# Kernel optimization log

Measured on AMD Instinct MI355X. Metric: run time of the kernel, lower is better.

Reference implementation:

```python
import jax, jax.numpy as jnp
import numpy as np

GROUPS = 32
NUM_HEADS = 8
EPS = 1e-5


def setup_inputs() -> dict:
    key = jax.random.key(0)
    ks = jax.random.split(key, 8)
    b, c, h, w = 2, 256, 64, 64
    x = jax.random.normal(ks[0], (b, c, h, w), dtype=jnp.float32)
    gn_w = jnp.ones((c,), dtype=jnp.float32)
    gn_b = jnp.zeros((c,), dtype=jnp.float32)
    qkv_w = jax.random.normal(ks[1], (3 * c, c), dtype=jnp.float32) * 0.02  # 1x1 conv
    qkv_b = jnp.zeros((3 * c,), dtype=jnp.float32)
    proj_w = jax.random.normal(ks[2], (c, c), dtype=jnp.float32) * 0.02  # 1x1 conv
    proj_b = jnp.zeros((c,), dtype=jnp.float32)
    return {"x": x, "gn_w": gn_w, "gn_b": gn_b, "qkv_w": qkv_w,
            "qkv_b": qkv_b, "proj_w": proj_w, "proj_b": proj_b}


def _group_norm(x, w, b):
    bsz, c, h, wd = x.shape
    xg = x.reshape(bsz, GROUPS, c // GROUPS, h * wd)
    mean = jnp.mean(xg, axis=(2, 3), keepdims=True)
    var = jnp.mean(jnp.square(xg - mean), axis=(2, 3), keepdims=True)
    xn = ((xg - mean) * jax.lax.rsqrt(var + EPS)).reshape(bsz, c, h, wd)
    return xn * w[None, :, None, None] + b[None, :, None, None]


def reference(x, gn_w, gn_b, qkv_w, qkv_b, proj_w, proj_b):
    b, c, h, w = x.shape
    hd = c // NUM_HEADS
    s = h * w
    xn = _group_norm(x, gn_w, gn_b)
    # 1x1 conv == channel matmul
    qkv = jnp.einsum('oc,bcs->bos', qkv_w, xn.reshape(b, c, s)) + qkv_b[None, :, None]
    qkv = qkv.reshape(b, 3, NUM_HEADS, hd, s)
    q, k, v = qkv[:, 0], qkv[:, 1], qkv[:, 2]  # (b, nh, hd, s)
    scale = 1.0 / jnp.sqrt(jnp.asarray(hd, dtype=x.dtype))
    scores = jnp.einsum('bhds,bhdt->bhst', q, k) * scale  # (b, nh, s, s)
    attn = jax.nn.softmax(scores, axis=-1)
    out = jnp.einsum('bhst,bhdt->bhds', attn, v)  # (b, nh, hd, s)
    out = out.reshape(b, c, h, w)
    out = jnp.einsum('oc,bcs->bos', proj_w, out.reshape(b, c, s)).reshape(b, c, h, w)
    out = out + proj_b[None, :, None, None]
    return out + x
```

## Files before the change

### kernel.cpp

```cpp
#include <hip/hip_runtime.h>
#include <hip/hip_bf16.h>

#define B_ 2
#define C_ 256
#define S_ 4096
#define NH 8
#define HD 32
#define EPSV 1e-5f
#define QSC2 0.25503487942324256f

typedef __bf16 bf16_t;
typedef bf16_t bf16x8 __attribute__((ext_vector_type(8)));
typedef float f32x4 __attribute__((ext_vector_type(4)));
typedef float f32x16 __attribute__((ext_vector_type(16)));
typedef int i32x2 __attribute__((ext_vector_type(2)));
typedef __hip_bfloat16 hbf;

__device__ inline unsigned cvtpk_bf16(float a, float b) {
  unsigned r;
  asm("v_cvt_pk_bf16_f32 %0, %1, %2" : "=v"(r) : "v"(a), "v"(b));
  return r;
}

#if __has_builtin(__builtin_amdgcn_exp2f)
#define EXP2R(x) __builtin_amdgcn_exp2f(x)
#else
#define EXP2R(x) exp2f(x)
#endif

__global__ __launch_bounds__(256) void prep_kernel(const float* __restrict__ qkv_w,
                                                   const float* __restrict__ proj_w,
                                                   const float* __restrict__ x,
                                                   hbf* __restrict__ qkv_wf, hbf* __restrict__ proj_wf,
                                                   float* __restrict__ stats) {
  int blk = blockIdx.x;
  if (blk < 128) {
    const float* src = (blk < 96) ? qkv_w : proj_w;
    hbf* dst = (blk < 96) ? qkv_wf : proj_wf;
    int i = (blk < 96 ? blk : blk - 96) * 256 + threadIdx.x;
    int nchunks = (blk < 96) ? 768 * 32 : 256 * 32;
    if (i < nchunks) {
      int o = i >> 5, c8 = (i & 31) * 8;
      alignas(16) hbf tmp[8];
#pragma unroll
      for (int j = 0; j < 8; j++) tmp[j] = __float2bfloat16(src[(size_t)o * C_ + c8 + j]);
      *(uint4*)&dst[(((size_t)(o >> 5) * 16) + (c8 >> 4)) * 512 + (o & 31) * 16 + (c8 & 15)] = *(uint4*)tmp;
    }
    return;
  }
  int sb = blk - 128;
  int bg = sb >> 3, chunk = sb & 7;
  const float4* xp4 = (const float4*)(x + (size_t)bg * 8 * S_);
  float sum = 0.f, sumsq = 0.f;
#pragma unroll
  for (int p = 0; p < 4; p++) {
    int i = threadIdx.x + p * 256;
    int ch = i >> 7, s4 = i & 127;
    float4 v = xp4[ch * (S_ >> 2) + chunk * 128 + s4];
    sum += v.x + v.y + v.z + v.w;
    sumsq += v.x * v.x + v.y * v.y + v.z * v.z + v.w * v.w;
  }
#pragma unroll
  for (int off = 32; off > 0; off >>= 1) {
    sum += __shfl_down(sum, off);
    sumsq += __shfl_down(sumsq, off);
  }
  __shared__ float red[2][4];
  int wid = threadIdx.x >> 6;
  if ((threadIdx.x & 63) == 0) { red[0][wid] = sum; red[1][wid] = sumsq; }
  __syncthreads();
  if (threadIdx.x == 0) {
    stats[sb * 2 + 0] = red[0][0] + red[0][1] + red[0][2] + red[0][3];
    stats[sb * 2 + 1] = red[1][0] + red[1][1] + red[1][2] + red[1][3];
  }
}

__global__ __launch_bounds__(256) void gn_apply(const float* __restrict__ x, const float* __restrict__ gw,
                                                const float* __restrict__ gb, const float* __restrict__ stats,
                                                hbf* __restrict__ xn) {
  int bg = blockIdx.x >> 3, chunk = blockIdx.x & 7;
  int b = bg >> 5, g = bg & 31;
  const float* xp = x + (size_t)bg * 8 * S_;
  float sum = 0.f, sumsq = 0.f;
#pragma unroll
  for (int k = 0; k < 8; k++) {
    sum += stats[(bg * 8 + k) * 2 + 0];
    sumsq += stats[(bg * 8 + k) * 2 + 1];
  }
  const float inv_n = 1.f / (8 * S_);
  float mean = sum * inv_n;
  float rstd = rsqrtf(fmaxf(sumsq * inv_n - mean * mean, 0.f) + EPSV);
  float scv[8], shv[8];
#pragma unroll
  for (int c = 0; c < 8; c++) {
    scv[c] = gw[g * 8 + c] * rstd;
    shv[c] = gb[g * 8 + c] - mean * scv[c];
  }
#pragma unroll
  for (int p = 0; p < 2; p++) {
    int s = chunk * 512 + p * 256 + threadIdx.x;
    alignas(16) hbf tmp[8];
#pragma unroll
    for (int c = 0; c < 8; c++)
      tmp[c] = __float2bfloat16(xp[(size_t)c * S_ + s] * scv[c] + shv[c]);
    *(uint4*)&xn[(((size_t)b * (S_ >> 5) + (s >> 5)) * 16 + (g >> 1)) * 512 + (s & 31) * 16 + (g & 1) * 8] =
        *(uint4*)tmp;
  }
}

__global__ __launch_bounds__(512, 4) void qkv_gemm(const hbf* __restrict__ xn, const hbf* __restrict__ wf,
                                                   const float* __restrict__ bias,
                                                   hbf* __restrict__ qbuf, hbf* __restrict__ kg,
                                                   hbf* __restrict__ vg) {
  int bt = blockIdx.z;
  int m0 = blockIdx.x * 128;
  int n0 = blockIdx.y * 128;
  int tid = threadIdx.x, lane = tid & 63, w = tid >> 6;
  int wq = w & 3, wo = w >> 2;
  int l31 = lane & 31, hi = lane >> 5;
  const int loff = l31 * 16 + hi * 8;
  const hbf* ap = xn + ((size_t)bt * (S_ >> 5) + (m0 >> 5) + wq) * 8192;
  int oc0 = n0 + wo * 64;
  const hbf* bp0 = wf + (size_t)(oc0 >> 5) * 8192;
  const hbf* bp1 = bp0 + 8192;
  f32x16 acc0 = {0.f,0.f,0.f,0.f,0.f,0.f,0.f,0.f,0.f,0.f,0.f,0.f,0.f,0.f,0.f,0.f};
  f32x16 acc1 = acc0;
#pragma unroll 4
  for (int ks = 0; ks < 16; ++ks) {
    bf16x8 af = *(const bf16x8*)(ap + ks * 512 + loff);
    bf16x8 b0 = *(const bf16x8*)(bp0 + ks * 512 + loff);
    bf16x8 b1 = *(const bf16x8*)(bp1 + ks * 512 + loff);
    acc0 = __builtin_amdgcn_mfma_f32_32x32x16_bf16(af, b0, acc0, 0, 0, 0);
    acc1 = __builtin_amdgcn_mfma_f32_32x32x16_bf16(af, b1, acc1, 0, 0, 0);
  }
  int s_base = m0 + wq * 32;
#pragma unroll
  for (int ct = 0; ct < 2; ++ct) {
    f32x16 a = ct ? acc1 : acc0;
    int oc = oc0 + ct * 32;
    int o = oc + l31;
    float bs = bias[o];
    if (oc < 256) {
#pragma unroll
      for (int r = 0; r < 16; r++) {
        int s = s_base + (r & 3) + 8 * (r >> 2) + 4 * hi;
        qbuf[((size_t)bt * S_ + s) * C_ + o] = __float2bfloat16((a[r] + bs) * QSC2);
      }
    } else if (oc < 512) {
      int hh = (oc - 256) >> 5;
      const size_t khead = (size_t)(bt * NH + hh) * (S_ >> 5);
#pragma unroll
      for (int r = 0; r < 16; r++) {
        int s = s_base + (r & 3) + 8 * (r >> 2) + 4 * hi;
        kg[(khead + (s >> 5)) * 1024 + (l31 >> 4) * 512 + (s & 31) * 16 + (l31 & 15)] =
            __float2bfloat16(a[r] + bs);
      }
    } else {
      int hh = (oc - 512) >> 5;
      const size_t vhead = (size_t)(bt * NH + hh) * (S_ >> 4);
#pragma unroll
      for (int r = 0; r < 16; r++) {
        int s = s_base + (r & 3) + 8 * (r >> 2) + 4 * hi;
        vg[(vhead + (s >> 4)) * 512 + l31 * 16 + (s & 15)] = __float2bfloat16(a[r] + bs);
      }
    }
  }
}

__device__ inline void softmax_pv(f32x16 sc, bf16x8 va0, bf16x8 va1,
                                  f32x16& o_acc, float& l_run) {
#pragma unroll
  for (int i = 0; i < 16; i++) sc[i] = EXP2R(sc[i]);
  {
    float s0a = sc[0] + sc[1], s1a = sc[2] + sc[3], s2a = sc[4] + sc[5], s3a = sc[6] + sc[7];
    float s4a = sc[8] + sc[9], s5a = sc[10] + sc[11], s6a = sc[12] + sc[13], s7a = sc[14] + sc[15];
    s0a += s1a; s2a += s3a; s4a += s5a; s6a += s7a;
    s0a += s2a; s4a += s6a;
    l_run += s0a + s4a;
  }
#pragma unroll
  for (int kb = 0; kb < 2; kb++) {
    unsigned a0 = cvtpk_bf16(sc[kb * 8 + 0], sc[kb * 8 + 1]);
    unsigned b0 = cvtpk_bf16(sc[kb * 8 + 2], sc[kb * 8 + 3]);
    unsigned a1 = cvtpk_bf16(sc[kb * 8 + 4], sc[kb * 8 + 5]);
    unsigned b1 = cvtpk_bf16(sc[kb * 8 + 6], sc[kb * 8 + 7]);
    i32x2 ra = __builtin_amdgcn_permlane32_swap((int)a0, (int)a1, false, false);
    i32x2 rb = __builtin_amdgcn_permlane32_swap((int)b0, (int)b1, false, false);
    union { unsigned u[4]; bf16x8 v; } pf;
    pf.u[0] = (unsigned)ra[0]; pf.u[1] = (unsigned)rb[0];
    pf.u[2] = (unsigned)ra[1]; pf.u[3] = (unsigned)rb[1];
    __builtin_amdgcn_s_setprio(1);
    o_acc = __builtin_amdgcn_mfma_f32_32x32x16_bf16(kb ? va1 : va0, pf.v, o_acc, 0, 0, 0);
    __builtin_amdgcn_s_setprio(0);
  }
}

__global__ __launch_bounds__(512, 4) void attn_kernel(const hbf* __restrict__ qbuf, const hbf* __restrict__ kg,
                                                      const hbf* __restrict__ vg, hbf* __restrict__ attn_t) {
  int bid = blockIdx.x;
  int xcd = bid & 7, idx = bid >> 3;
  int combo = (xcd << 1) | (idx >> 6);
  int bt = combo >> 3, h = combo & 7;
  int s0 = (idx & 63) << 6;
  int tid = threadIdx.x, lane = tid & 63, w = tid >> 6;
  int wq = w & 1, wt = w >> 1;
  int l31 = lane & 31, hi = lane >> 5;
  const int loff = (l31 << 4) + (hi << 3);
  int qrow = s0 + wq * 32 + l31;
  bf16x8 qf0 = *(const bf16x8*)&qbuf[((size_t)bt * S_ + qrow) * C_ + h * HD + hi * 8];
  bf16x8 qf1 = *(const bf16x8*)&qbuf[((size_t)bt * S_ + qrow) * C_ + h * HD + 16 + hi * 8];
  f32x16 o_acc = {0.f,0.f,0.f,0.f,0.f,0.f,0.f,0.f,0.f,0.f,0.f,0.f,0.f,0.f,0.f,0.f};
  const f32x16 z16 = o_acc;
  float l_run = 0.f;
  const int tq0 = wt << 10;
  const hbf* kq = kg + ((size_t)(bt * NH + h) * (S_ >> 5) + (tq0 >> 5)) * 1024;
  const hbf* vq = vg + ((size_t)(bt * NH + h) * (S_ >> 4) + (tq0 >> 4)) * 512;
  bf16x8 kaB0 = *(const bf16x8*)(kq + loff);
  bf16x8 kaB1 = *(const bf16x8*)(kq + loff + 512);
  f32x16 scA = __builtin_amdgcn_mfma_f32_32x32x16_bf16(kaB0, qf0, z16, 0, 0, 0);
  scA = __builtin_amdgcn_mfma_f32_32x32x16_bf16(kaB1, qf1, scA, 0, 0, 0);
  kaB0 = *(const bf16x8*)(kq + loff + 1024);
  kaB1 = *(const bf16x8*)(kq + loff + 1536);
  bf16x8 vaA0 = *(const bf16x8*)(vq + loff);
  bf16x8 vaA1 = *(const bf16x8*)(vq + loff + 512);
  kq += 2048;
  vq += 1024;
  for (int j = 0; j < 15; ++j) {
    bf16x8 vaB0 = *(const bf16x8*)(vq + loff);
    bf16x8 vaB1 = *(const bf16x8*)(vq + loff + 512);
    bf16x8 knA0 = *(const bf16x8*)(kq + loff);
    bf16x8 knA1 = *(const bf16x8*)(kq + loff + 512);
    __builtin_amdgcn_s_setprio(1);
    f32x16 scB = __builtin_amdgcn_mfma_f32_32x32x16_bf16(kaB0, qf0, z16, 0, 0, 0);
    scB = __builtin_amdgcn_mfma_f32_32x32x16_bf16(kaB1, qf1, scB, 0, 0, 0);
    __builtin_amdgcn_s_setprio(0);
    kaB0 = *(const bf16x8*)(kq + loff + 1024);
    kaB1 = *(const bf16x8*)(kq + loff + 1536);
    softmax_pv(scA, vaA0, vaA1, o_acc, l_run);
    vaA0 = *(const bf16x8*)(vq + loff + 1024);
    vaA1 = *(const bf16x8*)(vq + loff + 1536);
    __builtin_amdgcn_s_setprio(1);
    scA = __builtin_amdgcn_mfma_f32_32x32x16_bf16(knA0, qf0, z16, 0, 0, 0);
    scA = __builtin_amdgcn_mfma_f32_32x32x16_bf16(knA1, qf1, scA, 0, 0, 0);
    __builtin_amdgcn_s_setprio(0);
    softmax_pv(scB, vaB0, vaB1, o_acc, l_run);
    kq += 2048; vq += 2048;
  }
  {
    bf16x8 vaB0 = *(const bf16x8*)(vq + loff);
    bf16x8 vaB1 = *(const bf16x8*)(vq + loff + 512);
    f32x16 scB = __builtin_amdgcn_mfma_f32_32x32x16_bf16(kaB0, qf0, z16, 0, 0, 0);
    scB = __builtin_amdgcn_mfma_f32_32x32x16_bf16(kaB1, qf1, scB, 0, 0, 0);
    softmax_pv(scA, vaA0, vaA1, o_acc, l_run);
    softmax_pv(scB, vaB0, vaB1, o_acc, l_run);
  }
  __shared__ f32x16 ored[6 * 64];
  __shared__ float lred[8 * 64];
  __syncthreads();
  lred[(w << 6) + lane] = l_run;
  if (wt > 0) ored[((w - 2) << 6) + lane] = o_acc;
  __syncthreads();
  if (wt == 0) {
    float l_tot = 0.f;
#pragma unroll
    for (int k = 0; k < 4; k++) {
      int wp = wq + 2 * k;
      l_tot += lred[(wp << 6) + l31] + lred[(wp << 6) + 32 + l31];
    }
    f32x16 o = o_acc;
#pragma unroll
    for (int k = 0; k < 3; k++) {
      f32x16 t2 = ored[((wq + 2 * k) << 6) + lane];
#pragma unroll
      for (int i = 0; i < 16; i++) o[i] += t2[i];
    }
    float inv_l = 1.0f / l_tot;
#pragma unroll
    for (int c2 = 0; c2 < 4; c2++) {
      alignas(8) hbf tmp[4];
#pragma unroll
      for (int r = 0; r < 4; r++) tmp[r] = __float2bfloat16(o[c2 * 4 + r] * inv_l);
      *(uint2*)&attn_t[((size_t)bt * S_ + qrow) * C_ + h * HD + c2 * 8 + hi * 4] = *(uint2*)tmp;
    }
  }
}

__global__ __launch_bounds__(256) void proj_gemm(const hbf* __restrict__ attn_t, const hbf* __restrict__ wf,
                                                 const float* __restrict__ bias, const float* __restrict__ x,
                                                 float* __restrict__ out) {
  int bt = blockIdx.z;
  int s_blk = blockIdx.x * 64;
  int o_blk = blockIdx.y * 64;
  int tid = threadIdx.x, lane = tid & 63, w = tid >> 6;
  int wo = w & 1, ws = w >> 1;
  int l31 = lane & 31, hi = lane >> 5;
  const int loff = l31 * 16 + hi * 8;
  int o0 = o_blk + wo * 32;
  int s0 = s_blk + ws * 32;
  const hbf* ap = wf + (size_t)(o0 >> 5) * 8192;
  const hbf* bp = attn_t + ((size_t)bt * S_ + s0 + l31) * C_ + hi * 8;
  f32x16 acc = {0.f,0.f,0.f,0.f,0.f,0.f,0.f,0.f,0.f,0.f,0.f,0.f,0.f,0.f,0.f,0.f};
#pragma unroll 4
  for (int ks = 0; ks < 16; ++ks) {
    bf16x8 af = *(const bf16x8*)(ap + ks * 512 + loff);
    bf16x8 bf_ = *(const bf16x8*)(bp + ks * 16);
    acc = __builtin_amdgcn_mfma_f32_32x32x16_bf16(af, bf_, acc, 0, 0, 0);
  }
  int s = s0 + l31;
#pragma unroll
  for (int r = 0; r < 16; r++) {
    int o = o0 + (r & 3) + 8 * (r >> 2) + 4 * hi;
    size_t idx = ((size_t)bt * C_ + o) * S_ + s;
    out[idx] = acc[r] + bias[o] + x[idx];
  }
}

extern "C" void kernel_launch(void* const* d_in, const int* in_sizes, int n_in,
                              void* d_out, int out_size, void* d_ws, size_t ws_size,
                              hipStream_t stream) {
  const float* x = (const float*)d_in[0];
  const float* gn_w = (const float*)d_in[1];
  const float* gn_b = (const float*)d_in[2];
  const float* qkv_w = (const float*)d_in[3];
  const float* qkv_b = (const float*)d_in[4];
  const float* proj_w = (const float*)d_in[5];
  const float* proj_b = (const float*)d_in[6];
  float* out = (float*)d_out;

  hbf* qkv_wf = (hbf*)d_ws;
  hbf* proj_wf = qkv_wf + 768 * 256;
  hbf* xn = proj_wf + 256 * 256;
  hbf* qbuf = xn + (size_t)B_ * S_ * C_;
  hbf* kg = qbuf + (size_t)B_ * S_ * C_;
  hbf* vg = kg + (size_t)B_ * S_ * C_;
  hbf* attn_t = vg + (size_t)B_ * S_ * C_;
  float* stats = (float*)(attn_t + (size_t)B_ * S_ * C_);

  dim3 blk(256);
  prep_kernel<<<640, blk, 0, stream>>>(qkv_w, proj_w, x, qkv_wf, proj_wf, stats);
  gn_apply<<<512, blk, 0, stream>>>(x, gn_w, gn_b, stats, xn);
  qkv_gemm<<<dim3(32, 6, 2), dim3(512), 0, stream>>>(xn, qkv_wf, qkv_b, qbuf, kg, vg);
  attn_kernel<<<dim3(1024), dim3(512), 0, stream>>>(qbuf, kg, vg, attn_t);
  proj_gemm<<<dim3(64, 4, 2), blk, 0, stream>>>(attn_t, proj_wf, proj_b, x, out);
}
```

Measured before the change: 79.11 us.

## Fuse group-norm stats and apply into one kernel with inter-block atomic barrier

Merges the stats-reduction kernel and the group-norm apply kernel into one launch. The 8 blocks of each group publish partial sums, bump an atomic counter and spin until all 8 have arrived, then normalize their own chunk. This drops one kernel launch and re-reads x from cache instead of a separate pass. It adds a memset launch and relies on all 640 blocks being co-resident, or the spin could deadlock.

```diff
diff --git a/kernel.cpp b/kernel.cpp
--- a/kernel.cpp
+++ b/kernel.cpp
@@ -28,33 +28,36 @@
 #define EXP2R(x) exp2f(x)
 #endif
 
-__global__ __launch_bounds__(256) void prep_kernel(const float* __restrict__ qkv_w,
-                                                   const float* __restrict__ proj_w,
-                                                   const float* __restrict__ x,
-                                                   hbf* __restrict__ qkv_wf, hbf* __restrict__ proj_wf,
-                                                   float* __restrict__ stats) {
+__global__ __launch_bounds__(256) void gnw_fused(const float* __restrict__ qkv_w,
+                                                 const float* __restrict__ proj_w,
+                                                 const float* __restrict__ x,
+                                                 const float* __restrict__ gn_w,
+                                                 const float* __restrict__ gn_b,
+                                                 hbf* __restrict__ qkv_wf, hbf* __restrict__ proj_wf,
+                                                 float* __restrict__ stats, int* __restrict__ cnt,
+                                                 hbf* __restrict__ xn) {
   int blk = blockIdx.x;
+  int tid = threadIdx.x;
   if (blk < 128) {
     const float* src = (blk < 96) ? qkv_w : proj_w;
     hbf* dst = (blk < 96) ? qkv_wf : proj_wf;
-    int i = (blk < 96 ? blk : blk - 96) * 256 + threadIdx.x;
-    int nchunks = (blk < 96) ? 768 * 32 : 256 * 32;
-    if (i < nchunks) {
-      int o = i >> 5, c8 = (i & 31) * 8;
-      alignas(16) hbf tmp[8];
-#pragma unroll
-      for (int j = 0; j < 8; j++) tmp[j] = __float2bfloat16(src[(size_t)o * C_ + c8 + j]);
-      *(uint4*)&dst[(((size_t)(o >> 5) * 16) + (c8 >> 4)) * 512 + (o & 31) * 16 + (c8 & 15)] = *(uint4*)tmp;
-    }
+    int i = (blk < 96 ? blk : blk - 96) * 256 + tid;
+    int o = i >> 5, c8 = (i & 31) * 8;
+    alignas(16) hbf tmp[8];
+#pragma unroll
+    for (int j = 0; j < 8; j++) tmp[j] = __float2bfloat16(src[(size_t)o * C_ + c8 + j]);
+    *(uint4*)&dst[(((size_t)(o >> 5) * 16) + (c8 >> 4)) * 512 + (o & 31) * 16 + (c8 & 15)] = *(uint4*)tmp;
     return;
   }
   int sb = blk - 128;
   int bg = sb >> 3, chunk = sb & 7;
-  const float4* xp4 = (const float4*)(x + (size_t)bg * 8 * S_);
+  int b = bg >> 5, g = bg & 31;
+  const float* xp = x + (size_t)bg * 8 * S_;
+  const float4* xp4 = (const float4*)xp;
   float sum = 0.f, sumsq = 0.f;
 #pragma unroll
   for (int p = 0; p < 4; p++) {
-    int i = threadIdx.x + p * 256;
+    int i = tid + p * 256;
     int ch = i >> 7, s4 = i & 127;
     float4 v = xp4[ch * (S_ >> 2) + chunk * 128 + s4];
     sum += v.x + v.y + v.z + v.w;
@@ -66,39 +69,39 @@
     sumsq += __shfl_down(sumsq, off);
   }
   __shared__ float red[2][4];
-  int wid = threadIdx.x >> 6;
-  if ((threadIdx.x & 63) == 0) { red[0][wid] = sum; red[1][wid] = sumsq; }
+  __shared__ float bc[2];
+  int wid = tid >> 6;
+  if ((tid & 63) == 0) { red[0][wid] = sum; red[1][wid] = sumsq; }
   __syncthreads();
-  if (threadIdx.x == 0) {
+  if (tid == 0) {
     stats[sb * 2 + 0] = red[0][0] + red[0][1] + red[0][2] + red[0][3];
     stats[sb * 2 + 1] = red[1][0] + red[1][1] + red[1][2] + red[1][3];
-  }
-}
-
-__global__ __launch_bounds__(256) void gn_apply(const float* __restrict__ x, const float* __restrict__ gw,
-                                                const float* __restrict__ gb, const float* __restrict__ stats,
-                                                hbf* __restrict__ xn) {
-  int bg = blockIdx.x >> 3, chunk = blockIdx.x & 7;
-  int b = bg >> 5, g = bg & 31;
-  const float* xp = x + (size_t)bg * 8 * S_;
-  float sum = 0.f, sumsq = 0.f;
-#pragma unroll
-  for (int k = 0; k < 8; k++) {
-    sum += stats[(bg * 8 + k) * 2 + 0];
-    sumsq += stats[(bg * 8 + k) * 2 + 1];
-  }
-  const float inv_n = 1.f / (8 * S_);
-  float mean = sum * inv_n;
-  float rstd = rsqrtf(fmaxf(sumsq * inv_n - mean * mean, 0.f) + EPSV);
+    __threadfence();
+    __hip_atomic_fetch_add(&cnt[bg], 1, __ATOMIC_ACQ_REL, __HIP_MEMORY_SCOPE_AGENT);
+    while (__hip_atomic_load(&cnt[bg], __ATOMIC_ACQUIRE, __HIP_MEMORY_SCOPE_AGENT) < 8)
+      __builtin_amdgcn_s_sleep(2);
+    float ts = 0.f, tq = 0.f;
+#pragma unroll
+    for (int k = 0; k < 8; k++) {
+      ts += __hip_atomic_load(&stats[(bg * 8 + k) * 2 + 0], __ATOMIC_ACQUIRE, __HIP_MEMORY_SCOPE_AGENT);
+      tq += __hip_atomic_load(&stats[(bg * 8 + k) * 2 + 1], __ATOMIC_ACQUIRE, __HIP_MEMORY_SCOPE_AGENT);
+    }
+    const float inv_n = 1.f / (8 * S_);
+    float mean = ts * inv_n;
+    bc[0] = mean;
+    bc[1] = rsqrtf(fmaxf(tq * inv_n - mean * mean, 0.f) + EPSV);
+  }
+  __syncthreads();
+  float mean = bc[0], rstd = bc[1];
   float scv[8], shv[8];
 #pragma unroll
   for (int c = 0; c < 8; c++) {
-    scv[c] = gw[g * 8 + c] * rstd;
-    shv[c] = gb[g * 8 + c] - mean * scv[c];
+    scv[c] = gn_w[g * 8 + c] * rstd;
+    shv[c] = gn_b[g * 8 + c] - mean * scv[c];
   }
 #pragma unroll
   for (int p = 0; p < 2; p++) {
-    int s = chunk * 512 + p * 256 + threadIdx.x;
+    int s = chunk * 512 + p * 256 + tid;
     alignas(16) hbf tmp[8];
 #pragma unroll
     for (int c = 0; c < 8; c++)
@@ -335,10 +338,11 @@
   hbf* vg = kg + (size_t)B_ * S_ * C_;
   hbf* attn_t = vg + (size_t)B_ * S_ * C_;
   float* stats = (float*)(attn_t + (size_t)B_ * S_ * C_);
-
+  int* cnt = (int*)(stats + 64 * 8 * 2);
+
+  hipMemsetAsync(cnt, 0, 64 * sizeof(int), stream);
   dim3 blk(256);
-  prep_kernel<<<640, blk, 0, stream>>>(qkv_w, proj_w, x, qkv_wf, proj_wf, stats);
-  gn_apply<<<512, blk, 0, stream>>>(x, gn_w, gn_b, stats, xn);
+  gnw_fused<<<640, blk, 0, stream>>>(qkv_w, proj_w, x, gn_w, gn_b, qkv_wf, proj_wf, stats, cnt, xn);
   qkv_gemm<<<dim3(32, 6, 2), dim3(512), 0, stream>>>(xn, qkv_wf, qkv_b, qbuf, kg, vg);
   attn_kernel<<<dim3(1024), dim3(512), 0, stream>>>(qbuf, kg, vg, attn_t);
   proj_gemm<<<dim3(64, 4, 2), blk, 0, stream>>>(attn_t, proj_wf, proj_b, x, out);
```

Result: slower. 159.9 us (+102.2%).
